# Optimization experiments

Hardware: AMD Instinct MI355X
Metric: run time of the kernel (lower is better)

The kernel has to match this reference:

```python
import jax, jax.numpy as jnp
import numpy as np

N_NODES = 50000
N_EDGES = 800000
D = 128
N_LAYERS = 4
NUM_GRAPHS = 128
BN_EPS = 1e-5


def setup_inputs() -> dict:
    key = jax.random.key(0)
    ks = jax.random.split(key, 10)
    x = jax.random.normal(ks[0], (N_NODES, D), dtype=jnp.float32)
    edge_index = jax.random.randint(ks[1], (2, N_EDGES), 0, N_NODES, dtype=jnp.int64)
    batch = jnp.sort(jax.random.randint(ks[2], (N_NODES,), 0, NUM_GRAPHS, dtype=jnp.int64))
    # GINConv MLP params: Linear(D->D), ReLU, Linear(D->D); stacked over layers.
    scale = 1.0 / np.sqrt(D)
    W1 = jax.random.normal(ks[3], (N_LAYERS, D, D), dtype=jnp.float32) * scale
    b1 = jnp.zeros((N_LAYERS, D), dtype=jnp.float32)
    W2 = jax.random.normal(ks[4], (N_LAYERS, D, D), dtype=jnp.float32) * scale
    b2 = jnp.zeros((N_LAYERS, D), dtype=jnp.float32)
    eps = jnp.zeros((N_LAYERS,), dtype=jnp.float32)  # train_eps=True, init 0
    bn_gamma = jnp.ones((N_LAYERS - 1, D), dtype=jnp.float32)
    bn_beta = jnp.zeros((N_LAYERS - 1, D), dtype=jnp.float32)
    return {"x": x, "edge_index": edge_index, "batch": batch,
            "W1": W1, "b1": b1, "W2": W2, "b2": b2, "eps": eps,
            "bn_gamma": bn_gamma, "bn_beta": bn_beta}


def reference(x, edge_index, batch, W1, b1, W2, b2, eps, bn_gamma, bn_beta):
    src, dst = edge_index[0], edge_index[1]
    h = x
    for i in range(N_LAYERS):
        # GINConv: MLP((1+eps)*x_i + sum_{j->i} x_j)
        agg = jax.ops.segment_sum(h[src], dst, num_segments=N_NODES)  # [N, D]
        z = (1.0 + eps[i]) * h + agg
        z = jnp.maximum(z @ W1[i] + b1[i], 0.0) @ W2[i] + b2[i]
        if i < N_LAYERS - 1:
            # BatchNorm1d (training-mode batch statistics) + ReLU
            mu = jnp.mean(z, axis=0)
            var = jnp.var(z, axis=0)
            z = (z - mu) * jax.lax.rsqrt(var + BN_EPS) * bn_gamma[i] + bn_beta[i]
            z = jnp.maximum(z, 0.0)
        h = z
    # global_add_pool
    return jax.ops.segment_sum(h, batch, num_segments=NUM_GRAPHS)  # [G, D]
```

## Files before the change

### kernel.cpp

```cpp
#include <hip/hip_runtime.h>

#define N_NODES 50000
#define N_EDGES 800000
#define D 128
#define NUM_GRAPHS 128

typedef __attribute__((ext_vector_type(8)))  short bfrag8;
typedef __attribute__((ext_vector_type(16))) float f32x16;

__device__ __forceinline__ float4 f4zero() { return make_float4(0.f, 0.f, 0.f, 0.f); }

__device__ __forceinline__ unsigned short f2bf(float f) {
    unsigned u = __float_as_uint(f);
    unsigned r = (u + 0x7fffu + ((u >> 16) & 1u)) >> 16;
    return (unsigned short)r;
}
__device__ __forceinline__ float bf2f(unsigned short b) {
    return __uint_as_float(((unsigned)b) << 16);
}
__device__ __forceinline__ void acc8(float* a, uint4 r) {
    a[0] += __uint_as_float(r.x << 16);
    a[1] += __uint_as_float(r.x & 0xffff0000u);
    a[2] += __uint_as_float(r.y << 16);
    a[3] += __uint_as_float(r.y & 0xffff0000u);
    a[4] += __uint_as_float(r.z << 16);
    a[5] += __uint_as_float(r.z & 0xffff0000u);
    a[6] += __uint_as_float(r.w << 16);
    a[7] += __uint_as_float(r.w & 0xffff0000u);
}

__global__ __launch_bounds__(256) void prep_kernel(
    const float* __restrict__ W1, const float* __restrict__ W2,
    const float* __restrict__ x, short* __restrict__ Wt,
    ushort4* __restrict__ Hb, unsigned* __restrict__ HcDummy,
    int* __restrict__ deg, float* __restrict__ stats,
    float* __restrict__ outZero)
{
    int b = blockIdx.x, t = threadIdx.x;
    if (b < 512) {
        int idx = b * 256 + t;
        int m = idx >> 14, rem = idx & 16383;
        int k = rem >> 7, n = rem & 127;
        const float* W = (m < 4) ? (W1 + (size_t)m * 16384)
                                 : (W2 + (size_t)(m - 4) * 16384);
        Wt[(size_t)m * 16384 + n * 128 + k] = (short)f2bf(W[k * 128 + n]);
    } else if (b < 6762) {
        int i = (b - 512) * 256 + t;
        float4 v = ((const float4*)x)[i];
        Hb[i] = make_ushort4(f2bf(v.x), f2bf(v.y), f2bf(v.z), f2bf(v.w));
    } else if (b < 6958) {
        int i = (b - 6762) * 256 + t;
        if (i < N_NODES) deg[i] = 0;
    } else if (b < 6982) {
        int i = (b - 6958) * 256 + t;
        stats[i] = 0.f;
    } else if (b < 7046) {
        int i = (b - 6982) * 256 + t;
        outZero[i] = 0.f;
    } else {
        if (t < 64)       ((unsigned*)Hb)[(size_t)N_NODES * 64 + t] = 0u;
        else if (t < 128) HcDummy[t - 64] = 0u;
    }
}

__global__ __launch_bounds__(256) void hist_kernel(
    const int* __restrict__ dst, int* __restrict__ deg,
    unsigned short* __restrict__ edge_pos)
{
    int e = blockIdx.x * 256 + threadIdx.x;
    if (e < N_EDGES) edge_pos[e] = (unsigned short)atomicAdd(&deg[dst[e]], 1);
}

__global__ __launch_bounds__(256) void scan_block_kernel(
    const int* __restrict__ deg, int* __restrict__ row_ptr,
    int* __restrict__ blockSum)
{
    __shared__ int wsum[4];
    int t = threadIdx.x, b = blockIdx.x;
    int i = b * 256 + t;
    int v = (i < N_NODES) ? ((deg[i] + 7) & ~7) : 0;
    int lane = t & 63, wid = t >> 6;
    #pragma unroll
    for (int off = 1; off < 64; off <<= 1) {
        int u = __shfl_up(v, off, 64);
        if (lane >= off) v += u;
    }
    if (lane == 63) wsum[wid] = v;
    __syncthreads();
    int add = 0;
    for (int w = 0; w < wid; ++w) add += wsum[w];
    v += add;
    if (i < N_NODES) row_ptr[i + 1] = v;
    if (t == 255) blockSum[b] = v;
}

__global__ __launch_bounds__(256) void scan_fixup_kernel(
    const int* __restrict__ blockSum, int* __restrict__ row_ptr, int nb)
{
    __shared__ int wsum[4];
    __shared__ int sbuf[256];
    int t = threadIdx.x, b = blockIdx.x;
    int v = (t < nb) ? blockSum[t] : 0;
    int lane = t & 63, wid = t >> 6;
    #pragma unroll
    for (int off = 1; off < 64; off <<= 1) {
        int u = __shfl_up(v, off, 64);
        if (lane >= off) v += u;
    }
    if (lane == 63) wsum[wid] = v;
    __syncthreads();
    int add = 0;
    for (int w = 0; w < wid; ++w) add += wsum[w];
    sbuf[t] = v + add;
    __syncthreads();
    if (b == 0 && t == 0) row_ptr[0] = 0;
    if (b > 0) {
        int off = sbuf[b - 1];
        int i = b * 256 + t;
        if (i < N_NODES) row_ptr[i + 1] += off;
    }
}

__global__ __launch_bounds__(256) void fill_kernel(
    const int* __restrict__ src, const int* __restrict__ dst,
    const int* __restrict__ row_ptr, const unsigned short* __restrict__ edge_pos,
    const int* __restrict__ deg, unsigned short* __restrict__ csr_src)
{
    int b = blockIdx.x, t = threadIdx.x;
    if (b < 3125) {
        int e = b * 256 + t;
        if (e < N_EDGES)
            csr_src[row_ptr[dst[e]] + (int)edge_pos[e]] = (unsigned short)src[e];
    } else {
        int n = (b - 3125) * 256 + t;
        if (n < N_NODES) {
            int e0 = row_ptr[n] + deg[n];
            int e1 = row_ptr[n + 1];
            for (int j = e0; j < e1; ++j)
                csr_src[j] = (unsigned short)N_NODES;
        }
    }
}

__global__ __launch_bounds__(256) void bnapply_kernel(
    uint4* __restrict__ H, const float* __restrict__ stats,
    const float* __restrict__ gamma, const float* __restrict__ beta)
{
    __shared__ float sa[128], sb[128];
    int tid = threadIdx.x;
    if (tid < 128) {
        float s = 0.f, q = 0.f;
        #pragma unroll
        for (int k = 0; k < 8; ++k) {
            s += stats[k * 256 + tid];
            q += stats[k * 256 + 128 + tid];
        }
        const float invN = 1.0f / (float)N_NODES;
        float m = s * invN;
        float a = gamma[tid] * rsqrtf(q * invN - m * m + 1e-5f);
        sa[tid] = a;
        sb[tid] = beta[tid] - m * a;
    }
    __syncthreads();
    int id = blockIdx.x * 256 + tid;
    int c0 = (id & 15) * 8;
    uint4 u = H[id];
    float lo, hi;
    lo = fmaxf(sa[c0 + 0] * __uint_as_float(u.x << 16)          + sb[c0 + 0], 0.f);
    hi = fmaxf(sa[c0 + 1] * __uint_as_float(u.x & 0xffff0000u) + sb[c0 + 1], 0.f);
    u.x = (unsigned)f2bf(lo) | ((unsigned)f2bf(hi) << 16);
    lo = fmaxf(sa[c0 + 2] * __uint_as_float(u.y << 16)          + sb[c0 + 2], 0.f);
    hi = fmaxf(sa[c0 + 3] * __uint_as_float(u.y & 0xffff0000u) + sb[c0 + 3], 0.f);
    u.y = (unsigned)f2bf(lo) | ((unsigned)f2bf(hi) << 16);
    lo = fmaxf(sa[c0 + 4] * __uint_as_float(u.z << 16)          + sb[c0 + 4], 0.f);
    hi = fmaxf(sa[c0 + 5] * __uint_as_float(u.z & 0xffff0000u) + sb[c0 + 5], 0.f);
    u.z = (unsigned)f2bf(lo) | ((unsigned)f2bf(hi) << 16);
    lo = fmaxf(sa[c0 + 6] * __uint_as_float(u.w << 16)          + sb[c0 + 6], 0.f);
    hi = fmaxf(sa[c0 + 7] * __uint_as_float(u.w & 0xffff0000u) + sb[c0 + 7], 0.f);
    u.w = (unsigned)f2bf(lo) | ((unsigned)f2bf(hi) << 16);
    H[id] = u;
}

__global__ __launch_bounds__(256, 4) void layer_kernel(
    const ushort* __restrict__ Hin,
    const int* __restrict__ row_ptr,
    const unsigned short* __restrict__ csr,
    const float* __restrict__ epsp,
    const short* __restrict__ Wt1,
    const short* __restrict__ Wt2,
    const float* __restrict__ bias1,
    const float* __restrict__ bias2,
    ushort* __restrict__ Hout,
    float* __restrict__ statsBase,
    const int* __restrict__ batch,
    float* __restrict__ poolOut,
    int M)
{
    __shared__ __align__(16) short zlds[2][32 * 128];
    __shared__ float ssum[128];
    __shared__ float ssq[128];

    const int tid  = threadIdx.x;
    const int wv   = tid >> 6;
    const int lane = tid & 63;
    const int half = lane >> 5;
    const int ln   = lane & 31;
    const int rg   = wv & 1;
    const int ch   = wv >> 1;
    const int row0 = blockIdx.x * 64 + rg * 32;
    const bool doStats = (statsBase != nullptr);
    if (doStats && tid < 128) { ssum[tid] = 0.f; ssq[tid] = 0.f; }

    short* zw = &zlds[rg][0];

    {
        const uint4* H4 = (const uint4*)Hin;
        const float eps1 = 1.0f + *epsp;
        const int gl = tid & 15;
        #pragma unroll
        for (int it = 0; it < 4; ++it) {
            int r = it * 16 + (tid >> 4);
            int node = blockIdx.x * 64 + r;
            float acc[8] = {0.f, 0.f, 0.f, 0.f, 0.f, 0.f, 0.f, 0.f};
            if (node < M) {
                uint4 hv = H4[(size_t)node * 16 + gl];
                acc[0] = eps1 * __uint_as_float(hv.x << 16);
                acc[1] = eps1 * __uint_as_float(hv.x & 0xffff0000u);
                acc[2] = eps1 * __uint_as_float(hv.y << 16);
                acc[3] = eps1 * __uint_as_float(hv.y & 0xffff0000u);
                acc[4] = eps1 * __uint_as_float(hv.z << 16);
                acc[5] = eps1 * __uint_as_float(hv.z & 0xffff0000u);
                acc[6] = eps1 * __uint_as_float(hv.w << 16);
                acc[7] = eps1 * __uint_as_float(hv.w & 0xffff0000u);
                int beg = row_ptr[node], end = row_ptr[node + 1];
                int base = beg;
                int idx = (int)csr[base + gl];
                while (base < end) {
                    int nb = base + 16;
                    int nidx = 0;
                    if (nb < end) nidx = (int)csr[nb + gl];
                    int cnt = end - base;
                    int s0 = __shfl(idx, 0, 16), s1 = __shfl(idx, 1, 16);
                    int s2 = __shfl(idx, 2, 16), s3 = __shfl(idx, 3, 16);
                    int s4 = __shfl(idx, 4, 16), s5 = __shfl(idx, 5, 16);
                    int s6 = __shfl(idx, 6, 16), s7 = __shfl(idx, 7, 16);
                    uint4 u0 = H4[(size_t)s0 * 16 + gl];
                    uint4 u1 = H4[(size_t)s1 * 16 + gl];
                    uint4 u2 = H4[(size_t)s2 * 16 + gl];
                    uint4 u3 = H4[(size_t)s3 * 16 + gl];
                    uint4 u4 = H4[(size_t)s4 * 16 + gl];
                    uint4 u5 = H4[(size_t)s5 * 16 + gl];
                    uint4 u6 = H4[(size_t)s6 * 16 + gl];
                    uint4 u7 = H4[(size_t)s7 * 16 + gl];
                    if (cnt > 8) {
                        int t0 = __shfl(idx,  8, 16), t1 = __shfl(idx,  9, 16);
                        int t2 = __shfl(idx, 10, 16), t3 = __shfl(idx, 11, 16);
                        int t4 = __shfl(idx, 12, 16), t5 = __shfl(idx, 13, 16);
                        int t6 = __shfl(idx, 14, 16), t7 = __shfl(idx, 15, 16);
                        uint4 w0 = H4[(size_t)t0 * 16 + gl];
                        uint4 w1 = H4[(size_t)t1 * 16 + gl];
                        uint4 w2 = H4[(size_t)t2 * 16 + gl];
                        uint4 w3 = H4[(size_t)t3 * 16 + gl];
                        uint4 w4 = H4[(size_t)t4 * 16 + gl];
                        uint4 w5 = H4[(size_t)t5 * 16 + gl];
                        uint4 w6 = H4[(size_t)t6 * 16 + gl];
                        uint4 w7 = H4[(size_t)t7 * 16 + gl];
                        acc8(acc, u0); acc8(acc, u1); acc8(acc, u2); acc8(acc, u3);
                        acc8(acc, u4); acc8(acc, u5); acc8(acc, u6); acc8(acc, u7);
                        acc8(acc, w0); acc8(acc, w1); acc8(acc, w2); acc8(acc, w3);
                        acc8(acc, w4); acc8(acc, w5); acc8(acc, w6); acc8(acc, w7);
                    } else {
                        acc8(acc, u0); acc8(acc, u1); acc8(acc, u2); acc8(acc, u3);
                        acc8(acc, u4); acc8(acc, u5); acc8(acc, u6); acc8(acc, u7);
                    }
                    idx = nidx; base = nb;
                }
            }
            uint4 o;
            o.x = (unsigned)f2bf(acc[0]) | ((unsigned)f2bf(acc[1]) << 16);
            o.y = (unsigned)f2bf(acc[2]) | ((unsigned)f2bf(acc[3]) << 16);
            o.z = (unsigned)f2bf(acc[4]) | ((unsigned)f2bf(acc[5]) << 16);
            o.w = (unsigned)f2bf(acc[6]) | ((unsigned)f2bf(acc[7]) << 16);
            int rl = r & 31;
            ((uint4*)&zlds[r >> 5][0])[rl * 16 + (gl ^ (rl & 15))] = o;
        }
    }
    __syncthreads();

    bfrag8 af[8];
    #pragma unroll
    for (int kk = 0; kk < 8; ++kk) {
        int c = kk * 2 + half;
        af[kk] = *(const bfrag8*)(zw + ln * 128 + ((c ^ (ln & 15)) << 3));
    }
    __syncthreads();

    {
        f32x16 acc[2];
        #pragma unroll
        for (int ci = 0; ci < 2; ++ci)
            #pragma unroll
            for (int r = 0; r < 16; ++r) acc[ci][r] = 0.f;

        const short* Wb = Wt1 + (size_t)(ch * 64 + ln) * 128 + half * 8;
        #pragma unroll
        for (int kk = 0; kk < 8; ++kk) {
            #pragma unroll
            for (int ci = 0; ci < 2; ++ci) {
                bfrag8 bf = *(const bfrag8*)(Wb + ci * 32 * 128 + kk * 16);
                acc[ci] = __builtin_amdgcn_mfma_f32_32x32x16_bf16(
                    af[kk], bf, acc[ci], 0, 0, 0);
            }
        }
        #pragma unroll
        for (int ci = 0; ci < 2; ++ci) {
            int col = (ch * 2 + ci) * 32 + ln;
            int cc = col >> 3, co = col & 7;
            float bv = bias1[col];
            #pragma unroll
            for (int r = 0; r < 16; ++r) {
                int rloc = (r & 3) + 8 * (r >> 2) + 4 * half;
                float v = fmaxf(acc[ci][r] + bv, 0.f);
                zw[rloc * 128 + ((cc ^ (rloc & 15)) << 3) + co] = (short)f2bf(v);
            }
        }
    }
    __syncthreads();

    bfrag8 af2[8];
    #pragma unroll
    for (int kk = 0; kk < 8; ++kk) {
        int c = kk * 2 + half;
        af2[kk] = *(const bfrag8*)(zw + ln * 128 + ((c ^ (ln & 15)) << 3));
    }
    __syncthreads();

    {
        f32x16 acc[2];
        #pragma unroll
        for (int ci = 0; ci < 2; ++ci)
            #pragma unroll
            for (int r = 0; r < 16; ++r) acc[ci][r] = 0.f;

        const short* Wb = Wt2 + (size_t)(ch * 64 + ln) * 128 + half * 8;
        #pragma unroll
        for (int kk = 0; kk < 8; ++kk) {
            #pragma unroll
            for (int ci = 0; ci < 2; ++ci) {
                bfrag8 bf = *(const bfrag8*)(Wb + ci * 32 * 128 + kk * 16);
                acc[ci] = __builtin_amdgcn_mfma_f32_32x32x16_bf16(
                    af2[kk], bf, acc[ci], 0, 0, 0);
            }
        }
        #pragma unroll
        for (int ci = 0; ci < 2; ++ci) {
            int col = (ch * 2 + ci) * 32 + ln;
            int cc = col >> 3, co = col & 7;
            float bv = bias2[col];
            float s = 0.f, sq = 0.f;
            #pragma unroll
            for (int r = 0; r < 16; ++r) {
                int rloc = (r & 3) + 8 * (r >> 2) + 4 * half;
                float v = acc[ci][r] + bv;
                zw[rloc * 128 + ((cc ^ (rloc & 15)) << 3) + co] = (short)f2bf(v);
                if (row0 + rloc < M) { s += v; sq += v * v; }
            }
            if (doStats) {
                s  += __shfl_xor(s, 32);
                sq += __shfl_xor(sq, 32);
                if (half == 0) {
                    atomicAdd(&ssum[col], s);
                    atomicAdd(&ssq[col], sq);
                }
            }
        }
    }
    __syncthreads();

    if (poolOut == nullptr) {
        int4* Ho = (int4*)Hout;
        #pragma unroll
        for (int i = 0; i < 4; ++i) {
            int id = i * 256 + tid;
            int r = id >> 4, c = id & 15;
            int rl = r & 31;
            int grow = blockIdx.x * 64 + r;
            if (grow < M)
                Ho[(size_t)grow * 16 + c] =
                    ((const int4*)&zlds[r >> 5][0])[rl * 16 + (c ^ (rl & 15))];
        }
    } else {
        int c4 = tid & 31;
        int rl8 = tid >> 5;
        int cc = c4 >> 1, co = (c4 & 1) * 4;
        float4 ap = f4zero();
        int gcur = -1;
        for (int i = rl8; i < 64; i += 8) {
            int grow = blockIdx.x * 64 + i;
            if (grow >= M) break;
            int g = batch[grow];
            if (g != gcur) {
                if (gcur >= 0) {
                    float* o = poolOut + gcur * D + c4 * 4;
                    atomicAdd(o + 0, ap.x); atomicAdd(o + 1, ap.y);
                    atomicAdd(o + 2, ap.z); atomicAdd(o + 3, ap.w);
                }
                gcur = g; ap = f4zero();
            }
            const short* zr = &zlds[i >> 5][0];
            int rl = i & 31;
            const ushort4 u = *(const ushort4*)
                ((const ushort*)(zr + rl * 128 + ((cc ^ (rl & 15)) << 3) + co));
            ap.x += bf2f(u.x); ap.y += bf2f(u.y);
            ap.z += bf2f(u.z); ap.w += bf2f(u.w);
        }
        if (gcur >= 0) {
            float* o = poolOut + gcur * D + c4 * 4;
            atomicAdd(o + 0, ap.x); atomicAdd(o + 1, ap.y);
            atomicAdd(o + 2, ap.z); atomicAdd(o + 3, ap.w);
        }
    }
    if (doStats && tid < 128) {
        float* slot = statsBase + (size_t)(blockIdx.x & 7) * 256;
        atomicAdd(&slot[tid],       ssum[tid]);
        atomicAdd(&slot[128 + tid], ssq[tid]);
    }
}

extern "C" void kernel_launch(void* const* d_in, const int* in_sizes, int n_in,
                              void* d_out, int out_size, void* d_ws, size_t ws_size,
                              hipStream_t stream)
{
    const float* x     = (const float*)d_in[0];
    const int*   ei    = (const int*)d_in[1];
    const int*   batch = (const int*)d_in[2];
    const float* W1    = (const float*)d_in[3];
    const float* b1    = (const float*)d_in[4];
    const float* W2    = (const float*)d_in[5];
    const float* b2    = (const float*)d_in[6];
    const float* eps   = (const float*)d_in[7];
    const float* gamma = (const float*)d_in[8];
    const float* beta  = (const float*)d_in[9];
    float* out = (float*)d_out;

    unsigned short* Hb  = (unsigned short*)d_ws;
    unsigned short* Hc  = Hb + (size_t)(N_NODES + 1) * D;
    float* stats    = (float*)(Hc + (size_t)(N_NODES + 1) * D);
    int*   deg      = (int*)(stats + 3 * 2048);
    int*   row_ptr  = deg + N_NODES;
    int*   blockSum = row_ptr + N_NODES + 1;
    unsigned short* edge_pos = (unsigned short*)(blockSum + 256);
    unsigned short* csr_src  = edge_pos + N_EDGES;
    short* Wt       = (short*)(csr_src + N_EDGES + 7 * N_NODES + 16);

    const int* src = ei;
    const int* dst = ei + N_EDGES;

    const int edgeBlocks = (N_EDGES + 255) / 256;
    const int scanBlocks = (N_NODES + 255) / 256;
    const int bnBlocks   = (N_NODES * 16) / 256;
    const int gemmBlocks = (N_NODES + 63) / 64;

    prep_kernel<<<7047, 256, 0, stream>>>(W1, W2, x, Wt, (ushort4*)Hb,
                                          (unsigned*)(Hc + (size_t)N_NODES * D),
                                          deg, stats, out);
    hist_kernel<<<edgeBlocks, 256, 0, stream>>>(dst, deg, edge_pos);
    scan_block_kernel<<<scanBlocks, 256, 0, stream>>>(deg, row_ptr, blockSum);
    scan_fixup_kernel<<<scanBlocks, 256, 0, stream>>>(blockSum, row_ptr, scanBlocks);
    fill_kernel<<<edgeBlocks + scanBlocks, 256, 0, stream>>>(
        src, dst, row_ptr, edge_pos, deg, csr_src);

    unsigned short* Hin  = Hb;
    unsigned short* HoutB = Hc;
    for (int layer = 0; layer < 4; ++layer) {
        const bool bn = (layer < 3);
        if (layer > 0) {
            bnapply_kernel<<<bnBlocks, 256, 0, stream>>>(
                (uint4*)Hin, stats + (size_t)(layer - 1) * 2048,
                gamma + (size_t)(layer - 1) * D, beta + (size_t)(layer - 1) * D);
        }
        layer_kernel<<<gemmBlocks, 256, 0, stream>>>(
            Hin, row_ptr, csr_src, eps + layer,
            Wt + (size_t)layer * 16384, Wt + (size_t)(4 + layer) * 16384,
            b1 + (size_t)layer * D, b2 + (size_t)layer * D, HoutB,
            bn ? stats + (size_t)layer * 2048 : nullptr,
            bn ? nullptr : batch,
            bn ? nullptr : out, N_NODES);
        unsigned short* tmp = Hin; Hin = HoutB; HoutB = tmp;
    }
}
```

Baseline: 356.9 us.

## Shrink layer tile to 32 rows per block with four column-split waves

The fused layer kernel now processes 32 nodes per block instead of 64, with each of the four waves computing a 32-column slice and a single MFMA accumulator. This halves shared memory per block, doubles the block count for better load balance in the gather phase, and drops the shared-memory stats reduction in favour of direct global atomics from each wave. The trade-off is twice as many weight-fragment loads per node and more global atomic traffic on the BN statistic slots.

```diff
diff --git a/kernel.cpp b/kernel.cpp
--- a/kernel.cpp
+++ b/kernel.cpp
@@ -196,31 +196,26 @@
     float* __restrict__ poolOut,
     int M)
 {
-    __shared__ __align__(16) short zlds[2][32 * 128];
-    __shared__ float ssum[128];
-    __shared__ float ssq[128];
+    __shared__ __align__(16) short zlds[32 * 128];
 
     const int tid  = threadIdx.x;
-    const int wv   = tid >> 6;
     const int lane = tid & 63;
     const int half = lane >> 5;
     const int ln   = lane & 31;
-    const int rg   = wv & 1;
-    const int ch   = wv >> 1;
-    const int row0 = blockIdx.x * 64 + rg * 32;
+    const int ch   = tid >> 6;
+    const int row0 = blockIdx.x * 32;
     const bool doStats = (statsBase != nullptr);
-    if (doStats && tid < 128) { ssum[tid] = 0.f; ssq[tid] = 0.f; }
-
-    short* zw = &zlds[rg][0];
+
+    short* zw = &zlds[0];
 
     {
         const uint4* H4 = (const uint4*)Hin;
         const float eps1 = 1.0f + *epsp;
         const int gl = tid & 15;
         #pragma unroll
-        for (int it = 0; it < 4; ++it) {
+        for (int it = 0; it < 2; ++it) {
             int r = it * 16 + (tid >> 4);
-            int node = blockIdx.x * 64 + r;
+            int node = row0 + r;
             float acc[8] = {0.f, 0.f, 0.f, 0.f, 0.f, 0.f, 0.f, 0.f};
             if (node < M) {
                 uint4 hv = H4[(size_t)node * 16 + gl];
@@ -281,8 +276,7 @@
             o.y = (unsigned)f2bf(acc[2]) | ((unsigned)f2bf(acc[3]) << 16);
             o.z = (unsigned)f2bf(acc[4]) | ((unsigned)f2bf(acc[5]) << 16);
             o.w = (unsigned)f2bf(acc[6]) | ((unsigned)f2bf(acc[7]) << 16);
-            int rl = r & 31;
-            ((uint4*)&zlds[r >> 5][0])[rl * 16 + (gl ^ (rl & 15))] = o;
+            ((uint4*)zlds)[r * 16 + (gl ^ (r & 15))] = o;
         }
     }
     __syncthreads();
@@ -296,33 +290,24 @@
     __syncthreads();
 
     {
-        f32x16 acc[2];
-        #pragma unroll
-        for (int ci = 0; ci < 2; ++ci)
-            #pragma unroll
-            for (int r = 0; r < 16; ++r) acc[ci][r] = 0.f;
-
-        const short* Wb = Wt1 + (size_t)(ch * 64 + ln) * 128 + half * 8;
+        f32x16 acc;
+        #pragma unroll
+        for (int r = 0; r < 16; ++r) acc[r] = 0.f;
+
+        const short* Wb = Wt1 + (size_t)(ch * 32 + ln) * 128 + half * 8;
         #pragma unroll
         for (int kk = 0; kk < 8; ++kk) {
-            #pragma unroll
-            for (int ci = 0; ci < 2; ++ci) {
-                bfrag8 bf = *(const bfrag8*)(Wb + ci * 32 * 128 + kk * 16);
-                acc[ci] = __builtin_amdgcn_mfma_f32_32x32x16_bf16(
-                    af[kk], bf, acc[ci], 0, 0, 0);
-            }
-        }
-        #pragma unroll
-        for (int ci = 0; ci < 2; ++ci) {
-            int col = (ch * 2 + ci) * 32 + ln;
-            int cc = col >> 3, co = col & 7;
-            float bv = bias1[col];
-            #pragma unroll
-            for (int r = 0; r < 16; ++r) {
-                int rloc = (r & 3) + 8 * (r >> 2) + 4 * half;
-                float v = fmaxf(acc[ci][r] + bv, 0.f);
-                zw[rloc * 128 + ((cc ^ (rloc & 15)) << 3) + co] = (short)f2bf(v);
-            }
+            bfrag8 bf = *(const bfrag8*)(Wb + kk * 16);
+            acc = __builtin_amdgcn_mfma_f32_32x32x16_bf16(af[kk], bf, acc, 0, 0, 0);
+        }
+        int col = ch * 32 + ln;
+        int cc = col >> 3, co = col & 7;
+        float bv = bias1[col];
+        #pragma unroll
+        for (int r = 0; r < 16; ++r) {
+            int rloc = (r & 3) + 8 * (r >> 2) + 4 * half;
+            float v = fmaxf(acc[r] + bv, 0.f);
+            zw[rloc * 128 + ((cc ^ (rloc & 15)) << 3) + co] = (short)f2bf(v);
         }
     }
     __syncthreads();
@@ -336,42 +321,34 @@
     __syncthreads();
 
     {
-        f32x16 acc[2];
-        #pragma unroll
-        for (int ci = 0; ci < 2; ++ci)
-            #pragma unroll
-            for (int r = 0; r < 16; ++r) acc[ci][r] = 0.f;
-
-        const short* Wb = Wt2 + (size_t)(ch * 64 + ln) * 128 + half * 8;
+        f32x16 acc;
+        #pragma unroll
+        for (int r = 0; r < 16; ++r) acc[r] = 0.f;
+
+        const short* Wb = Wt2 + (size_t)(ch * 32 + ln) * 128 + half * 8;
         #pragma unroll
         for (int kk = 0; kk < 8; ++kk) {
-            #pragma unroll
-            for (int ci = 0; ci < 2; ++ci) {
-                bfrag8 bf = *(const bfrag8*)(Wb + ci * 32 * 128 + kk * 16);
-                acc[ci] = __builtin_amdgcn_mfma_f32_32x32x16_bf16(
-                    af2[kk], bf, acc[ci], 0, 0, 0);
-            }
-        }
-        #pragma unroll
-        for (int ci = 0; ci < 2; ++ci) {
-            int col = (ch * 2 + ci) * 32 + ln;
-            int cc = col >> 3, co = col & 7;
-            float bv = bias2[col];
-            float s = 0.f, sq = 0.f;
-            #pragma unroll
-            for (int r = 0; r < 16; ++r) {
-                int rloc = (r & 3) + 8 * (r >> 2) + 4 * half;
-                float v = acc[ci][r] + bv;
-                zw[rloc * 128 + ((cc ^ (rloc & 15)) << 3) + co] = (short)f2bf(v);
-                if (row0 + rloc < M) { s += v; sq += v * v; }
-            }
-            if (doStats) {
-                s  += __shfl_xor(s, 32);
-                sq += __shfl_xor(sq, 32);
-                if (half == 0) {
-                    atomicAdd(&ssum[col], s);
-                    atomicAdd(&ssq[col], sq);
-                }
+            bfrag8 bf = *(const bfrag8*)(Wb + kk * 16);
+            acc = __builtin_amdgcn_mfma_f32_32x32x16_bf16(af2[kk], bf, acc, 0, 0, 0);
+        }
+        int col = ch * 32 + ln;
+        int cc = col >> 3, co = col & 7;
+        float bv = bias2[col];
+        float s = 0.f, sq = 0.f;
+        #pragma unroll
+        for (int r = 0; r < 16; ++r) {
+            int rloc = (r & 3) + 8 * (r >> 2) + 4 * half;
+            float v = acc[r] + bv;
+            zw[rloc * 128 + ((cc ^ (rloc & 15)) << 3) + co] = (short)f2bf(v);
+            if (row0 + rloc < M) { s += v; sq += v * v; }
+        }
+        if (doStats) {
+            s  += __shfl_xor(s, 32);
+            sq += __shfl_xor(sq, 32);
+            if (half == 0) {
+                float* slot = statsBase + (size_t)(blockIdx.x & 7) * 256;
+                atomicAdd(&slot[col],       s);
+                atomicAdd(&slot[128 + col], sq);
             }
         }
     }
@@ -380,14 +357,13 @@
     if (poolOut == nullptr) {
         int4* Ho = (int4*)Hout;
         #pragma unroll
-        for (int i = 0; i < 4; ++i) {
+        for (int i = 0; i < 2; ++i) {
             int id = i * 256 + tid;
             int r = id >> 4, c = id & 15;
-            int rl = r & 31;
-            int grow = blockIdx.x * 64 + r;
+            int grow = row0 + r;
             if (grow < M)
                 Ho[(size_t)grow * 16 + c] =
-                    ((const int4*)&zlds[r >> 5][0])[rl * 16 + (c ^ (rl & 15))];
+                    ((const int4*)zlds)[r * 16 + (c ^ (r & 15))];
         }
     } else {
         int c4 = tid & 31;
@@ -395,8 +371,8 @@
         int cc = c4 >> 1, co = (c4 & 1) * 4;
         float4 ap = f4zero();
         int gcur = -1;
-        for (int i = rl8; i < 64; i += 8) {
-            int grow = blockIdx.x * 64 + i;
+        for (int i = rl8; i < 32; i += 8) {
+            int grow = row0 + i;
             if (grow >= M) break;
             int g = batch[grow];
             if (g != gcur) {
@@ -407,10 +383,8 @@
                 }
                 gcur = g; ap = f4zero();
             }
-            const short* zr = &zlds[i >> 5][0];
-            int rl = i & 31;
             const ushort4 u = *(const ushort4*)
-                ((const ushort*)(zr + rl * 128 + ((cc ^ (rl & 15)) << 3) + co));
+                ((const ushort*)(zw + i * 128 + ((cc ^ (i & 15)) << 3) + co));
             ap.x += bf2f(u.x); ap.y += bf2f(u.y);
             ap.z += bf2f(u.z); ap.w += bf2f(u.w);
         }
@@ -419,11 +393,6 @@
             atomicAdd(o + 0, ap.x); atomicAdd(o + 1, ap.y);
             atomicAdd(o + 2, ap.z); atomicAdd(o + 3, ap.w);
         }
-    }
-    if (doStats && tid < 128) {
-        float* slot = statsBase + (size_t)(blockIdx.x & 7) * 256;
-        atomicAdd(&slot[tid],       ssum[tid]);
-        atomicAdd(&slot[128 + tid], ssq[tid]);
     }
 }
 
@@ -459,7 +428,7 @@
     const int edgeBlocks = (N_EDGES + 255) / 256;
     const int scanBlocks = (N_NODES + 255) / 256;
     const int bnBlocks   = (N_NODES * 16) / 256;
-    const int gemmBlocks = (N_NODES + 63) / 64;
+    const int gemmBlocks = (N_NODES + 31) / 32;
 
     prep_kernel<<<7047, 256, 0, stream>>>(W1, W2, x, Wt, (ushort4*)Hb,
                                           (unsigned*)(Hc + (size_t)N_NODES * D),
```

Measured after the change: 360.1 us. About the same (+0.9%).

## Fuse BatchNorm apply and ReLU into neighbor gather of next layer

Applied to the files above, without the earlier changes.

Drops the separate bnapply kernel and applies the previous layer's BN affine transform and ReLU on the fly to every gathered neighbor row and to the self row inside the layer kernel. Padded CSR entries point to a zero sentinel row that now picks up the BN shift, so a count-based correction subtracts their contribution. This removes a full read and write pass over H and three launches, at the cost of extra FMA/max per gathered element (about 16x more elementwise work). It also switches CSR index loads and H stores to nontemporal hints, and BN is now applied in fp32 without re-rounding to bf16.

```diff
diff --git a/kernel.cpp b/kernel.cpp
--- a/kernel.cpp
+++ b/kernel.cpp
@@ -7,6 +7,7 @@
 
 typedef __attribute__((ext_vector_type(8)))  short bfrag8;
 typedef __attribute__((ext_vector_type(16))) float f32x16;
+typedef __attribute__((ext_vector_type(4)))  int   intv4;
 
 __device__ __forceinline__ float4 f4zero() { return make_float4(0.f, 0.f, 0.f, 0.f); }
 
@@ -18,15 +19,17 @@
 __device__ __forceinline__ float bf2f(unsigned short b) {
     return __uint_as_float(((unsigned)b) << 16);
 }
-__device__ __forceinline__ void acc8(float* a, uint4 r) {
-    a[0] += __uint_as_float(r.x << 16);
-    a[1] += __uint_as_float(r.x & 0xffff0000u);
-    a[2] += __uint_as_float(r.y << 16);
-    a[3] += __uint_as_float(r.y & 0xffff0000u);
-    a[4] += __uint_as_float(r.z << 16);
-    a[5] += __uint_as_float(r.z & 0xffff0000u);
-    a[6] += __uint_as_float(r.w << 16);
-    a[7] += __uint_as_float(r.w & 0xffff0000u);
+__device__ __forceinline__ void acc8bn(float* a, uint4 r,
+                                       const float* sa, const float* sb,
+                                       float flo) {
+    a[0] += fmaxf(fmaf(sa[0], __uint_as_float(r.x << 16),          sb[0]), flo);
+    a[1] += fmaxf(fmaf(sa[1], __uint_as_float(r.x & 0xffff0000u), sb[1]), flo);
+    a[2] += fmaxf(fmaf(sa[2], __uint_as_float(r.y << 16),          sb[2]), flo);
+    a[3] += fmaxf(fmaf(sa[3], __uint_as_float(r.y & 0xffff0000u), sb[3]), flo);
+    a[4] += fmaxf(fmaf(sa[4], __uint_as_float(r.z << 16),          sb[4]), flo);
+    a[5] += fmaxf(fmaf(sa[5], __uint_as_float(r.z & 0xffff0000u), sb[5]), flo);
+    a[6] += fmaxf(fmaf(sa[6], __uint_as_float(r.w << 16),          sb[6]), flo);
+    a[7] += fmaxf(fmaf(sa[7], __uint_as_float(r.w & 0xffff0000u), sb[7]), flo);
 }
 
 __global__ __launch_bounds__(256) void prep_kernel(
@@ -142,50 +145,15 @@
     }
 }
 
-__global__ __launch_bounds__(256) void bnapply_kernel(
-    uint4* __restrict__ H, const float* __restrict__ stats,
-    const float* __restrict__ gamma, const float* __restrict__ beta)
-{
-    __shared__ float sa[128], sb[128];
-    int tid = threadIdx.x;
-    if (tid < 128) {
-        float s = 0.f, q = 0.f;
-        #pragma unroll
-        for (int k = 0; k < 8; ++k) {
-            s += stats[k * 256 + tid];
-            q += stats[k * 256 + 128 + tid];
-        }
-        const float invN = 1.0f / (float)N_NODES;
-        float m = s * invN;
-        float a = gamma[tid] * rsqrtf(q * invN - m * m + 1e-5f);
-        sa[tid] = a;
-        sb[tid] = beta[tid] - m * a;
-    }
-    __syncthreads();
-    int id = blockIdx.x * 256 + tid;
-    int c0 = (id & 15) * 8;
-    uint4 u = H[id];
-    float lo, hi;
-    lo = fmaxf(sa[c0 + 0] * __uint_as_float(u.x << 16)          + sb[c0 + 0], 0.f);
-    hi = fmaxf(sa[c0 + 1] * __uint_as_float(u.x & 0xffff0000u) + sb[c0 + 1], 0.f);
-    u.x = (unsigned)f2bf(lo) | ((unsigned)f2bf(hi) << 16);
-    lo = fmaxf(sa[c0 + 2] * __uint_as_float(u.y << 16)          + sb[c0 + 2], 0.f);
-    hi = fmaxf(sa[c0 + 3] * __uint_as_float(u.y & 0xffff0000u) + sb[c0 + 3], 0.f);
-    u.y = (unsigned)f2bf(lo) | ((unsigned)f2bf(hi) << 16);
-    lo = fmaxf(sa[c0 + 4] * __uint_as_float(u.z << 16)          + sb[c0 + 4], 0.f);
-    hi = fmaxf(sa[c0 + 5] * __uint_as_float(u.z & 0xffff0000u) + sb[c0 + 5], 0.f);
-    u.z = (unsigned)f2bf(lo) | ((unsigned)f2bf(hi) << 16);
-    lo = fmaxf(sa[c0 + 6] * __uint_as_float(u.w << 16)          + sb[c0 + 6], 0.f);
-    hi = fmaxf(sa[c0 + 7] * __uint_as_float(u.w & 0xffff0000u) + sb[c0 + 7], 0.f);
-    u.w = (unsigned)f2bf(lo) | ((unsigned)f2bf(hi) << 16);
-    H[id] = u;
-}
-
 __global__ __launch_bounds__(256, 4) void layer_kernel(
     const ushort* __restrict__ Hin,
     const int* __restrict__ row_ptr,
     const unsigned short* __restrict__ csr,
+    const int* __restrict__ deg,
     const float* __restrict__ epsp,
+    const float* __restrict__ statsPrev,
+    const float* __restrict__ gammaP,
+    const float* __restrict__ betaP,
     const short* __restrict__ Wt1,
     const short* __restrict__ Wt2,
     const float* __restrict__ bias1,
@@ -199,6 +167,8 @@
     __shared__ __align__(16) short zlds[2][32 * 128];
     __shared__ float ssum[128];
     __shared__ float ssq[128];
+    __shared__ float salds[128];
+    __shared__ float sblds[128];
 
     const int tid  = threadIdx.x;
     const int wv   = tid >> 6;
@@ -211,12 +181,39 @@
     const bool doStats = (statsBase != nullptr);
     if (doStats && tid < 128) { ssum[tid] = 0.f; ssq[tid] = 0.f; }
 
+    if (tid < 128) {
+        float a = 1.f, bb = 0.f;
+        if (statsPrev) {
+            float s = 0.f, q = 0.f;
+            #pragma unroll
+            for (int k = 0; k < 8; ++k) {
+                s += statsPrev[k * 256 + tid];
+                q += statsPrev[k * 256 + 128 + tid];
+            }
+            const float invN = 1.0f / (float)N_NODES;
+            float m = s * invN;
+            a = gammaP[tid] * rsqrtf(q * invN - m * m + 1e-5f);
+            bb = betaP[tid] - m * a;
+        }
+        salds[tid] = a;
+        sblds[tid] = bb;
+    }
+    __syncthreads();
+
+    const float flo = statsPrev ? 0.f : -3.0e38f;
+
     short* zw = &zlds[rg][0];
 
     {
         const uint4* H4 = (const uint4*)Hin;
         const float eps1 = 1.0f + *epsp;
         const int gl = tid & 15;
+        float sa8[8], sb8[8];
+        #pragma unroll
+        for (int j = 0; j < 8; ++j) {
+            sa8[j] = salds[gl * 8 + j];
+            sb8[j] = sblds[gl * 8 + j];
+        }
         #pragma unroll
         for (int it = 0; it < 4; ++it) {
             int r = it * 16 + (tid >> 4);
@@ -224,21 +221,18 @@
             float acc[8] = {0.f, 0.f, 0.f, 0.f, 0.f, 0.f, 0.f, 0.f};
             if (node < M) {
                 uint4 hv = H4[(size_t)node * 16 + gl];
-                acc[0] = eps1 * __uint_as_float(hv.x << 16);
-                acc[1] = eps1 * __uint_as_float(hv.x & 0xffff0000u);
-                acc[2] = eps1 * __uint_as_float(hv.y << 16);
-                acc[3] = eps1 * __uint_as_float(hv.y & 0xffff0000u);
-                acc[4] = eps1 * __uint_as_float(hv.z << 16);
-                acc[5] = eps1 * __uint_as_float(hv.z & 0xffff0000u);
-                acc[6] = eps1 * __uint_as_float(hv.w << 16);
-                acc[7] = eps1 * __uint_as_float(hv.w & 0xffff0000u);
+                acc8bn(acc, hv, sa8, sb8, flo);
+                #pragma unroll
+                for (int j = 0; j < 8; ++j) acc[j] *= eps1;
+
                 int beg = row_ptr[node], end = row_ptr[node + 1];
                 int base = beg;
-                int idx = (int)csr[base + gl];
+                int idx = (int)__builtin_nontemporal_load(&csr[base + gl]);
                 while (base < end) {
                     int nb = base + 16;
                     int nidx = 0;
-                    if (nb < end) nidx = (int)csr[nb + gl];
+                    if (nb < end)
+                        nidx = (int)__builtin_nontemporal_load(&csr[nb + gl]);
                     int cnt = end - base;
                     int s0 = __shfl(idx, 0, 16), s1 = __shfl(idx, 1, 16);
                     int s2 = __shfl(idx, 2, 16), s3 = __shfl(idx, 3, 16);
@@ -265,15 +259,28 @@
                         uint4 w5 = H4[(size_t)t5 * 16 + gl];
                         uint4 w6 = H4[(size_t)t6 * 16 + gl];
                         uint4 w7 = H4[(size_t)t7 * 16 + gl];
-                        acc8(acc, u0); acc8(acc, u1); acc8(acc, u2); acc8(acc, u3);
-                        acc8(acc, u4); acc8(acc, u5); acc8(acc, u6); acc8(acc, u7);
-                        acc8(acc, w0); acc8(acc, w1); acc8(acc, w2); acc8(acc, w3);
-                        acc8(acc, w4); acc8(acc, w5); acc8(acc, w6); acc8(acc, w7);
+                        acc8bn(acc, u0, sa8, sb8, flo); acc8bn(acc, u1, sa8, sb8, flo);
+                        acc8bn(acc, u2, sa8, sb8, flo); acc8bn(acc, u3, sa8, sb8, flo);
+                        acc8bn(acc, u4, sa8, sb8, flo); acc8bn(acc, u5, sa8, sb8, flo);
+                        acc8bn(acc, u6, sa8, sb8, flo); acc8bn(acc, u7, sa8, sb8, flo);
+                        acc8bn(acc, w0, sa8, sb8, flo); acc8bn(acc, w1, sa8, sb8, flo);
+                        acc8bn(acc, w2, sa8, sb8, flo); acc8bn(acc, w3, sa8, sb8, flo);
+                        acc8bn(acc, w4, sa8, sb8, flo); acc8bn(acc, w5, sa8, sb8, flo);
+                        acc8bn(acc, w6, sa8, sb8, flo); acc8bn(acc, w7, sa8, sb8, flo);
                     } else {
-                        acc8(acc, u0); acc8(acc, u1); acc8(acc, u2); acc8(acc, u3);
-                        acc8(acc, u4); acc8(acc, u5); acc8(acc, u6); acc8(acc, u7);
+                        acc8bn(acc, u0, sa8, sb8, flo); acc8bn(acc, u1, sa8, sb8, flo);
+                        acc8bn(acc, u2, sa8, sb8, flo); acc8bn(acc, u3, sa8, sb8, flo);
+                        acc8bn(acc, u4, sa8, sb8, flo); acc8bn(acc, u5, sa8, sb8, flo);
+                        acc8bn(acc, u6, sa8, sb8, flo); acc8bn(acc, u7, sa8, sb8, flo);
                     }
                     idx = nidx; base = nb;
+                }
+                int npad = (end - beg) - deg[node];
+                if (npad > 0) {
+                    float fp = (float)npad;
+                    #pragma unroll
+                    for (int j = 0; j < 8; ++j)
+                        acc[j] -= fp * fmaxf(sb8[j], flo);
                 }
             }
             uint4 o;
@@ -378,16 +385,17 @@
     __syncthreads();
 
     if (poolOut == nullptr) {
-        int4* Ho = (int4*)Hout;
+        intv4* Ho = (intv4*)Hout;
         #pragma unroll
         for (int i = 0; i < 4; ++i) {
             int id = i * 256 + tid;
             int r = id >> 4, c = id & 15;
             int rl = r & 31;
             int grow = blockIdx.x * 64 + r;
-            if (grow < M)
-                Ho[(size_t)grow * 16 + c] =
-                    ((const int4*)&zlds[r >> 5][0])[rl * 16 + (c ^ (rl & 15))];
+            if (grow < M) {
+                intv4 v = ((const intv4*)&zlds[r >> 5][0])[rl * 16 + (c ^ (rl & 15))];
+                __builtin_nontemporal_store(v, &Ho[(size_t)grow * 16 + c]);
+            }
         }
     } else {
         int c4 = tid & 31;
@@ -458,7 +466,6 @@
 
     const int edgeBlocks = (N_EDGES + 255) / 256;
     const int scanBlocks = (N_NODES + 255) / 256;
-    const int bnBlocks   = (N_NODES * 16) / 256;
     const int gemmBlocks = (N_NODES + 63) / 64;
 
     prep_kernel<<<7047, 256, 0, stream>>>(W1, W2, x, Wt, (ushort4*)Hb,
@@ -474,13 +481,12 @@
     unsigned short* HoutB = Hc;
     for (int layer = 0; layer < 4; ++layer) {
         const bool bn = (layer < 3);
-        if (layer > 0) {
-            bnapply_kernel<<<bnBlocks, 256, 0, stream>>>(
-                (uint4*)Hin, stats + (size_t)(layer - 1) * 2048,
-                gamma + (size_t)(layer - 1) * D, beta + (size_t)(layer - 1) * D);
-        }
+        const float* statsPrev = (layer > 0) ? stats + (size_t)(layer - 1) * 2048
+                                             : nullptr;
+        int gl = (layer > 0) ? layer - 1 : 0;
         layer_kernel<<<gemmBlocks, 256, 0, stream>>>(
-            Hin, row_ptr, csr_src, eps + layer,
+            Hin, row_ptr, csr_src, deg, eps + layer,
+            statsPrev, gamma + (size_t)gl * D, beta + (size_t)gl * D,
             Wt + (size_t)layer * 16384, Wt + (size_t)(4 + layer) * 16384,
             b1 + (size_t)layer * D, b2 + (size_t)layer * D, HoutB,
             bn ? stats + (size_t)layer * 2048 : nullptr,
```

Result: slower. 407.4 us (+14.1%).
